# Kernel tuning notes

Hardware: AMD Instinct MI355X
Metric: run time of the kernel (lower is better)

Reference implementation:

```python
import jax, jax.numpy as jnp
import numpy as np

B, C, H, W = 4, 512, 128, 256
INNER = 128
HEADS = 4
GROUPS = 32
EPS = 1e-5


def _ln(x, w, b):
    m = x.mean(-1, keepdims=True)
    v = jnp.var(x, axis=-1, keepdims=True)
    return (x - m) * jax.lax.rsqrt(v + EPS) * w + b


def _mhsa(x, wq, wk, wv, ln_w, ln_b):
    # x: (Bn, N, Ci); torch Linear: y = x @ W.T
    Bn, N, Ci = x.shape
    d = Ci // HEADS
    xn = _ln(x, ln_w, ln_b)
    q = (xn @ wq.T).reshape(Bn, N, HEADS, d).transpose(0, 2, 1, 3)
    k = (xn @ wk.T).reshape(Bn, N, HEADS, d).transpose(0, 2, 1, 3)
    v = (xn @ wv.T).reshape(Bn, N, HEADS, d).transpose(0, 2, 1, 3)
    attn = jax.nn.softmax(jnp.einsum('bhnd,bhmd->bhnm', q, k) * (d ** -0.5), axis=-1)
    out = jnp.einsum('bhnm,bhmd->bhnd', attn, v).transpose(0, 2, 1, 3).reshape(Bn, N, Ci)
    return out


def setup_inputs() -> dict:
    key = jax.random.key(0)
    ks = jax.random.split(key, 10)
    s = 0.02
    return {
        'x': jax.random.normal(ks[0], (B, C, H, W), jnp.float32),
        'proj_in_w': jax.random.normal(ks[1], (INNER, C), jnp.float32) * s,
        't_q_w': jax.random.normal(ks[2], (INNER, INNER), jnp.float32) * s,
        't_k_w': jax.random.normal(ks[3], (INNER, INNER), jnp.float32) * s,
        't_v_w': jax.random.normal(ks[4], (INNER, INNER), jnp.float32) * s,
        't_norm_w': jnp.ones((INNER,), jnp.float32),
        't_norm_b': jnp.zeros((INNER,), jnp.float32),
        'f_q_w': jax.random.normal(ks[5], (INNER, INNER), jnp.float32) * s,
        'f_k_w': jax.random.normal(ks[6], (INNER, INNER), jnp.float32) * s,
        'f_v_w': jax.random.normal(ks[7], (INNER, INNER), jnp.float32) * s,
        'f_norm_w': jnp.ones((INNER,), jnp.float32),
        'f_norm_b': jnp.zeros((INNER,), jnp.float32),
        'proj_out_w': jax.random.normal(ks[8], (C, INNER), jnp.float32) * s,
        'gn_w': jnp.ones((C,), jnp.float32),
        'gn_b': jnp.zeros((C,), jnp.float32),
    }


def reference(x, proj_in_w, t_q_w, t_k_w, t_v_w, t_norm_w, t_norm_b,
              f_q_w, f_k_w, f_v_w, f_norm_w, f_norm_b,
              proj_out_w, gn_w, gn_b):
    Bx, Cx, Hx, Wx = x.shape
    inner = proj_in_w.shape[0]
    # 1x1 conv in
    z = jnp.einsum('bchw,oc->bohw', x, proj_in_w)
    # row-wise (temporal) attention: sequences of length Wx
    t_in = z.transpose(0, 2, 3, 1).reshape(Bx * Hx, Wx, inner)
    t_out = t_in + _mhsa(t_in, t_q_w, t_k_w, t_v_w, t_norm_w, t_norm_b)
    t_out = t_out.reshape(Bx, Hx, Wx, inner).transpose(0, 3, 1, 2)  # (B, inner, H, W)
    # col-wise (frequency) attention: sequences of length Hx
    f_in = t_out.transpose(0, 3, 2, 1).reshape(Bx * Wx, Hx, inner)
    f_out = f_in + _mhsa(f_in, f_q_w, f_k_w, f_v_w, f_norm_w, f_norm_b)
    f_out = f_out.reshape(Bx, Wx, Hx, inner).transpose(0, 3, 2, 1)  # (B, inner, H, W)
    # 1x1 conv out
    out = jnp.einsum('bihw,oi->bohw', f_out, proj_out_w)
    # GroupNorm(32, C)
    og = out.reshape(Bx, GROUPS, Cx // GROUPS, Hx, Wx)
    m = og.mean(axis=(2, 3, 4), keepdims=True)
    v = jnp.var(og, axis=(2, 3, 4), keepdims=True)
    og = (og - m) * jax.lax.rsqrt(v + EPS)
    out = og.reshape(Bx, Cx, Hx, Wx) * gn_w[None, :, None, None] + gn_b[None, :, None, None]
    return x + out
```

## Files before the change

kernel.cpp:

```cpp
#include <hip/hip_runtime.h>
#include <cstdint>

typedef __bf16 bf16;
typedef __attribute__((ext_vector_type(8))) __bf16 bf16x8;
typedef __attribute__((ext_vector_type(4))) __bf16 bf16x4;
typedef __attribute__((ext_vector_type(4))) float f32x4;

static __device__ __forceinline__ f32x4 mfma16(bf16x8 a, bf16x8 b, f32x4 c) {
    return __builtin_amdgcn_mfma_f32_16x16x32_bf16(a, b, c, 0, 0, 0);
}
static __device__ __forceinline__ bf16x4 cvt4(f32x4 v) {
    bf16x4 r; r[0]=(bf16)v[0]; r[1]=(bf16)v[1]; r[2]=(bf16)v[2]; r[3]=(bf16)v[3]; return r;
}

__global__ __launch_bounds__(256) void k_proj_in(
    const float* __restrict__ x, const float* __restrict__ Wi, bf16* __restrict__ z)
{
    __shared__ bf16 As[128][72];
    __shared__ bf16 Bs[64][72];
    const int tid = threadIdx.x;
    const int lane = tid & 63, w = tid >> 6;
    const int ll = lane & 15, lg = lane >> 4;
    const int b = blockIdx.x >> 9;
    const int n0 = (blockIdx.x & 511) * 64;
    const float* xb = x + (size_t)b * 512 * 32768;

    f32x4 acc[2][4];
    const f32x4 Z4 = {0.f,0.f,0.f,0.f};
    #pragma unroll
    for (int i=0;i<2;i++) { acc[i][0]=Z4; acc[i][1]=Z4; acc[i][2]=Z4; acc[i][3]=Z4; }

    for (int c0 = 0; c0 < 512; c0 += 64) {
        #pragma unroll
        for (int r = 0; r < 8; ++r) {
            int idx = r*256 + tid;
            int o = idx >> 4, cq = idx & 15;
            f32x4 v = *(const f32x4*)(Wi + (size_t)o*512 + c0 + cq*4);
            *(bf16x4*)&As[o][cq*4] = cvt4(v);
        }
        #pragma unroll
        for (int r = 0; r < 4; ++r) {
            int idx = r*256 + tid;
            int k = idx >> 4, nq = idx & 15;
            f32x4 v = *(const f32x4*)(xb + (size_t)(c0 + k)*32768 + n0 + nq*4);
            #pragma unroll
            for (int j=0;j<4;j++) Bs[nq*4+j][k] = (bf16)v[j];
        }
        __syncthreads();
        #pragma unroll
        for (int ks = 0; ks < 2; ++ks) {
            bf16x8 af[2], bfr[4];
            #pragma unroll
            for (int mt=0;mt<2;mt++) af[mt]  = *(const bf16x8*)&As[w*32+mt*16+ll][ks*32+lg*8];
            #pragma unroll
            for (int nt=0;nt<4;nt++) bfr[nt] = *(const bf16x8*)&Bs[nt*16+ll][ks*32+lg*8];
            #pragma unroll
            for (int mt=0;mt<2;mt++)
                #pragma unroll
                for (int nt=0;nt<4;nt++)
                    acc[mt][nt] = mfma16(af[mt], bfr[nt], acc[mt][nt]);
        }
        __syncthreads();
    }
    #pragma unroll
    for (int mt=0;mt<2;mt++)
      #pragma unroll
      for (int nt=0;nt<4;nt++) {
        int o0 = w*32 + mt*16 + lg*4;
        int token = b*32768 + n0 + nt*16 + ll;
        *(bf16x4*)&z[(size_t)token*128 + o0] = cvt4(acc[mt][nt]);
      }
}

__global__ __launch_bounds__(256) void k_qkv(
    const bf16* __restrict__ zin, const float* __restrict__ lnw, const float* __restrict__ lnb,
    const float* __restrict__ Wq, const float* __restrict__ Wk, const float* __restrict__ Wv,
    bf16* __restrict__ Qb, bf16* __restrict__ Kb, bf16* __restrict__ Vt, int nshift)
{
    __shared__ bf16 xs[64][136];
    __shared__ bf16 wsm[128][136];
    const int tid = threadIdx.x;
    const int lane = tid & 63, w = tid >> 6;
    const int ll = lane & 15, lg = lane >> 4;
    const int t0 = blockIdx.x * 64;
    const int N = 1 << nshift;

    {
        const int sub = tid & 15;
        float wv[8], bv[8];
        #pragma unroll
        for (int j=0;j<8;j++){ wv[j]=lnw[sub*8+j]; bv[j]=lnb[sub*8+j]; }
        #pragma unroll
        for (int r=0;r<4;r++){
            int tl = r*16 + (tid >> 4);
            bf16x8 v = *(const bf16x8*)&zin[(size_t)(t0+tl)*128 + sub*8];
            float f[8]; float sm=0.f, ssq=0.f;
            #pragma unroll
            for (int j=0;j<8;j++){ f[j]=(float)v[j]; sm+=f[j]; ssq+=f[j]*f[j]; }
            #pragma unroll
            for (int d=1; d<16; d<<=1){ sm += __shfl_xor(sm,d); ssq += __shfl_xor(ssq,d); }
            float mean = sm*(1.f/128.f);
            float var  = ssq*(1.f/128.f) - mean*mean;
            float rr = rsqrtf(var + 1e-5f);
            bf16x8 ov;
            #pragma unroll
            for (int j=0;j<8;j++) ov[j] = (bf16)((f[j]-mean)*rr*wv[j] + bv[j]);
            *(bf16x8*)&xs[tl][sub*8] = ov;
        }
    }

    const float* Wm[3] = {Wq, Wk, Wv};
    const f32x4 Z4 = {0.f,0.f,0.f,0.f};
    for (int m = 0; m < 3; ++m) {
        __syncthreads();
        const float scale = (m == 0) ? 0.25503486f : 1.0f;
        #pragma unroll
        for (int r=0;r<16;r++){
            int idx = r*256 + tid;
            int o = idx >> 5, q = idx & 31;
            f32x4 v = *(const f32x4*)(Wm[m] + (size_t)o*128 + q*4);
            v[0]*=scale; v[1]*=scale; v[2]*=scale; v[3]*=scale;
            *(bf16x4*)&wsm[o][q*4] = cvt4(v);
        }
        __syncthreads();
        f32x4 acc[4][2];
        #pragma unroll
        for (int i=0;i<4;i++){ acc[i][0]=Z4; acc[i][1]=Z4; }
        #pragma unroll
        for (int ks=0; ks<4; ++ks){
            bf16x8 xa[4], wb[2];
            #pragma unroll
            for (int tt=0;tt<4;tt++) xa[tt] = *(const bf16x8*)&xs[tt*16+ll][ks*32+lg*8];
            #pragma unroll
            for (int ot=0;ot<2;ot++) wb[ot] = *(const bf16x8*)&wsm[w*32+ot*16+ll][ks*32+lg*8];
            if (m < 2) {
                #pragma unroll
                for (int tt=0;tt<4;tt++)
                    #pragma unroll
                    for (int ot=0;ot<2;ot++)
                        acc[tt][ot] = mfma16(xa[tt], wb[ot], acc[tt][ot]);
            } else {
                #pragma unroll
                for (int tt=0;tt<4;tt++)
                    #pragma unroll
                    for (int ot=0;ot<2;ot++)
                        acc[tt][ot] = mfma16(wb[ot], xa[tt], acc[tt][ot]);
            }
        }
        if (m < 2) {
            bf16* dst = (m==0) ? Qb : Kb;
            #pragma unroll
            for (int tt=0;tt<4;tt++)
              #pragma unroll
              for (int ot=0;ot<2;ot++)
                #pragma unroll
                for (int r=0;r<4;r++){
                    int token = t0 + tt*16 + lg*4 + r;
                    int sq = token >> nshift, n = token & (N-1);
                    int dk = ot*16 + ll;
                    dst[((size_t)(sq*4 + w)*N + n)*32 + dk] = (bf16)acc[tt][ot][r];
                }
        } else {
            #pragma unroll
            for (int tt=0;tt<4;tt++)
              #pragma unroll
              for (int ot=0;ot<2;ot++)
                #pragma unroll
                for (int r=0;r<4;r++){
                    int dk = ot*16 + lg*4 + r;
                    int token = t0 + tt*16 + ll;
                    int sq = token >> nshift, n = token & (N-1);
                    Vt[((size_t)(sq*4 + w)*32 + dk)*N + n] = (bf16)acc[tt][ot][r];
                }
        }
    }
}

template<int N>
__global__ __launch_bounds__(256, 2) void k_attn(
    const bf16* __restrict__ Qb, const bf16* __restrict__ Kb, const bf16* __restrict__ Vt,
    const bf16* __restrict__ tin, bf16* __restrict__ tout, int spb_shift)
{
    constexpr int T = N/16;
    constexpr int NQT = N/64;
    constexpr int VP = N + 8;
    __shared__ bf16 Ks[N][40];
    __shared__ bf16 Vs[32][VP];
    const int tid = threadIdx.x;
    const int lane = tid & 63, w = tid >> 6;
    const int ll = lane & 15, lg = lane >> 4;
    const int sh = blockIdx.x;
    const int s = sh >> 2, h = sh & 3;
    const size_t base = (size_t)sh * N * 32;

    #pragma unroll
    for (int r=0;r<N/64;r++){
        int idx = r*256 + tid;
        int n = idx >> 2, c = idx & 3;
        *(bf16x8*)&Ks[n][c*8] = *(const bf16x8*)&Kb[base + (size_t)n*32 + c*8];
    }
    #pragma unroll
    for (int r=0;r<N/64;r++){
        int idx = r*256 + tid;
        int dd = idx / (N/8), nc = idx % (N/8);
        *(bf16x8*)&Vs[dd][nc*8] = *(const bf16x8*)&Vt[base + (size_t)dd*N + nc*8];
    }
    bf16x8 qf[NQT];
    #pragma unroll
    for (int qt=0;qt<NQT;qt++)
        qf[qt] = *(const bf16x8*)&Qb[base + (size_t)(w*(N/4) + qt*16 + ll)*32 + lg*8];
    __syncthreads();

    const f32x4 Z4 = {0.f,0.f,0.f,0.f};
    f32x4 Oacc[NQT][2];
    float smv[NQT];

    #pragma unroll
    for (int qt=0; qt<NQT; ++qt){
        f32x4 sc[T];
        #pragma unroll
        for (int t=0;t<T;t++){
            bf16x8 kf = *(const bf16x8*)&Ks[t*16+ll][lg*8];
            sc[t] = mfma16(kf, qf[qt], Z4);
        }
        float mx = sc[0][0];
        #pragma unroll
        for (int t=0;t<T;t++)
            #pragma unroll
            for (int r=0;r<4;r++) mx = fmaxf(mx, sc[t][r]);
        mx = fmaxf(mx, __shfl_xor(mx, 16));
        mx = fmaxf(mx, __shfl_xor(mx, 32));
        float sm = 0.f;
        #pragma unroll
        for (int t=0;t<T;t++){
            #pragma unroll
            for (int r=0;r<4;r++){ float p = exp2f(sc[t][r] - mx); sc[t][r] = p; sm += p; }
        }
        sm += __shfl_xor(sm, 16);
        sm += __shfl_xor(sm, 32);
        smv[qt] = sm;

        f32x4 O0 = Z4, O1 = Z4;
        #pragma unroll
        for (int ks=0; ks<N/32; ++ks){
            bf16x4 pa = cvt4(sc[2*ks]), pb = cvt4(sc[2*ks+1]);
            bf16x8 pf;
            #pragma unroll
            for (int j=0;j<4;j++){ pf[j] = pa[j]; pf[4+j] = pb[j]; }
            bf16x4 a0 = *(const bf16x4*)&Vs[ll][ks*32 + lg*4];
            bf16x4 a1 = *(const bf16x4*)&Vs[ll][ks*32 + lg*4 + 16];
            bf16x4 b0 = *(const bf16x4*)&Vs[16+ll][ks*32 + lg*4];
            bf16x4 b1 = *(const bf16x4*)&Vs[16+ll][ks*32 + lg*4 + 16];
            bf16x8 v0, v1;
            #pragma unroll
            for (int j=0;j<4;j++){ v0[j]=a0[j]; v0[4+j]=a1[j]; v1[j]=b0[j]; v1[4+j]=b1[j]; }
            O0 = mfma16(v0, pf, O0);
            O1 = mfma16(v1, pf, O1);
        }
        Oacc[qt][0] = O0; Oacc[qt][1] = O1;
    }

    __syncthreads();
    #pragma unroll
    for (int qt=0; qt<NQT; ++qt){
        float inv = 1.f / smv[qt];
        int q = w*(N/4) + qt*16 + ll;
        #pragma unroll
        for (int dt=0; dt<2; ++dt){
            bf16x4 o4;
            #pragma unroll
            for (int r=0;r<4;r++) o4[r] = (bf16)(Oacc[qt][dt][r]*inv);
            *(bf16x4*)&Ks[q][dt*16 + lg*4] = o4;
        }
    }
    __syncthreads();
    const int spb_mask = (1 << spb_shift) - 1;
    #pragma unroll
    for (int it=0; it<N/64; ++it){
        int q = it*64 + (tid >> 2);
        int part = tid & 3;
        size_t ti = ((size_t)(s*N + q))*128 + h*32 + part*8;
        size_t to = ((size_t)((((s >> spb_shift)*N + q) << spb_shift) + (s & spb_mask)))*128 + h*32 + part*8;
        bf16x8 a = *(const bf16x8*)&Ks[q][part*8];
        bf16x8 rs = *(const bf16x8*)&tin[ti];
        bf16x8 o;
        #pragma unroll
        for (int j=0;j<8;j++) o[j] = (bf16)((float)a[j] + (float)rs[j]);
        *(bf16x8*)&tout[to] = o;
    }
}

__global__ __launch_bounds__(256) void k_gnsum(
    const bf16* __restrict__ f, const float* __restrict__ Wo, float* __restrict__ part)
{
    __shared__ bf16 As[128][136];
    __shared__ bf16 Bs[64][136];
    const int tid = threadIdx.x;
    const int lane = tid & 63, w = tid >> 6;
    const int ll = lane & 15, lg = lane >> 4;
    const int b  = blockIdx.x >> 11;
    const int ms = (blockIdx.x >> 9) & 3;
    const int ns = blockIdx.x & 511;
    const int n0 = ns*64, o0 = ms*128;

    #pragma unroll
    for (int r=0;r<16;r++){
        int idx = r*256 + tid;
        int o = idx >> 5, q = idx & 31;
        f32x4 v = *(const f32x4*)(Wo + (size_t)(o0+o)*128 + q*4);
        *(bf16x4*)&As[o][q*4] = cvt4(v);
    }
    #pragma unroll
    for (int r=0;r<4;r++){
        int idx = r*256 + tid;
        int nl = idx >> 4, ch = idx & 15;
        *(bf16x8*)&Bs[nl][ch*8] = *(const bf16x8*)&f[(size_t)(b*32768 + n0 + nl)*128 + ch*8];
    }
    __syncthreads();
    const f32x4 Z4 = {0.f,0.f,0.f,0.f};
    f32x4 acc[2][4];
    #pragma unroll
    for (int i=0;i<2;i++){ acc[i][0]=Z4; acc[i][1]=Z4; acc[i][2]=Z4; acc[i][3]=Z4; }
    #pragma unroll
    for (int ks=0;ks<4;ks++){
        bf16x8 af[2], bfr[4];
        #pragma unroll
        for (int mt=0;mt<2;mt++) af[mt]  = *(const bf16x8*)&As[w*32+mt*16+ll][ks*32+lg*8];
        #pragma unroll
        for (int nt=0;nt<4;nt++) bfr[nt] = *(const bf16x8*)&Bs[nt*16+ll][ks*32+lg*8];
        #pragma unroll
        for (int mt=0;mt<2;mt++)
            #pragma unroll
            for (int nt=0;nt<4;nt++)
                acc[mt][nt] = mfma16(af[mt], bfr[nt], acc[mt][nt]);
    }
    #pragma unroll
    for (int mt=0;mt<2;mt++){
        float ps=0.f, pss=0.f;
        #pragma unroll
        for (int nt=0;nt<4;nt++)
            #pragma unroll
            for (int r=0;r<4;r++){ float v = acc[mt][nt][r]; ps += v; pss += v*v; }
        #pragma unroll
        for (int d=1; d<64; d<<=1){ ps += __shfl_xor(ps,d); pss += __shfl_xor(pss,d); }
        if (lane == 0){
            int g = ms*8 + w*2 + mt;
            size_t pi = ((size_t)(b*32+g)*512 + ns)*2;
            part[pi] = ps; part[pi+1] = pss;
        }
    }
}

__global__ __launch_bounds__(256) void k_gnstat(
    const float* __restrict__ part, float* __restrict__ stats)
{
    const int bg = blockIdx.x;
    float s = 0.f, ss = 0.f;
    for (int i = threadIdx.x; i < 512; i += 256) {
        s  += part[((size_t)bg*512 + i)*2];
        ss += part[((size_t)bg*512 + i)*2 + 1];
    }
    #pragma unroll
    for (int d=1; d<64; d<<=1){ s += __shfl_xor(s,d); ss += __shfl_xor(ss,d); }
    __shared__ float sh[8];
    const int w = threadIdx.x >> 6;
    if ((threadIdx.x & 63) == 0) { sh[w*2] = s; sh[w*2+1] = ss; }
    __syncthreads();
    if (threadIdx.x == 0) {
        float S = sh[0]+sh[2]+sh[4]+sh[6], SS = sh[1]+sh[3]+sh[5]+sh[7];
        float mean = S * (1.f/524288.f);
        float var  = SS * (1.f/524288.f) - mean*mean;
        stats[bg*2]   = mean;
        stats[bg*2+1] = rsqrtf(var + 1e-5f);
    }
}

__global__ __launch_bounds__(256) void k_apply(
    const bf16* __restrict__ f, const float* __restrict__ Wo, const float* __restrict__ x,
    const float* __restrict__ stats, const float* __restrict__ gw, const float* __restrict__ gb,
    float* __restrict__ out)
{
    __shared__ bf16 As[128][136];
    __shared__ bf16 Bs[64][136];
    const int tid = threadIdx.x;
    const int lane = tid & 63, w = tid >> 6;
    const int ll = lane & 15, lg = lane >> 4;
    const int b  = blockIdx.x >> 11;
    const int ms = (blockIdx.x >> 9) & 3;
    const int ns = blockIdx.x & 511;
    const int n0 = ns*64, o0 = ms*128;

    #pragma unroll
    for (int r=0;r<16;r++){
        int idx = r*256 + tid;
        int o = idx >> 5, q = idx & 31;
        f32x4 v = *(const f32x4*)(Wo + (size_t)(o0+o)*128 + q*4);
        *(bf16x4*)&As[o][q*4] = cvt4(v);
    }
    #pragma unroll
    for (int r=0;r<4;r++){
        int idx = r*256 + tid;
        int nl = idx >> 4, ch = idx & 15;
        *(bf16x8*)&Bs[nl][ch*8] = *(const bf16x8*)&f[(size_t)(b*32768 + n0 + nl)*128 + ch*8];
    }
    __syncthreads();
    const f32x4 Z4 = {0.f,0.f,0.f,0.f};
    f32x4 acc[2][4];
    #pragma unroll
    for (int i=0;i<2;i++){ acc[i][0]=Z4; acc[i][1]=Z4; acc[i][2]=Z4; acc[i][3]=Z4; }
    #pragma unroll
    for (int ks=0;ks<4;ks++){
        bf16x8 af[2], bfr[4];
        #pragma unroll
        for (int mt=0;mt<2;mt++) af[mt]  = *(const bf16x8*)&As[w*32+mt*16+ll][ks*32+lg*8];
        #pragma unroll
        for (int nt=0;nt<4;nt++) bfr[nt] = *(const bf16x8*)&Bs[nt*16+ll][ks*32+lg*8];
        #pragma unroll
        for (int mt=0;mt<2;mt++)
            #pragma unroll
            for (int nt=0;nt<4;nt++)
                acc[mt][nt] = mfma16(af[mt], bfr[nt], acc[mt][nt]);
    }
    __syncthreads();
    float* Od = (float*)&As[0][0];
    #pragma unroll
    for (int mt=0;mt<2;mt++){
        int g = ms*8 + w*2 + mt;
        float mean = stats[(b*32+g)*2];
        float rstd = stats[(b*32+g)*2+1];
        #pragma unroll
        for (int r=0;r<4;r++){
            int o_l = w*32 + mt*16 + lg*4 + r;
            float sw = rstd * gw[o0 + o_l];
            float sb = gb[o0 + o_l] - mean*sw;
            #pragma unroll
            for (int nt=0;nt<4;nt++)
                Od[o_l*68 + nt*16 + ll] = acc[mt][nt][r]*sw + sb;
        }
    }
    __syncthreads();
    #pragma unroll
    for (int it=0; it<8; ++it){
        int idx = it*256 + tid;
        int o_l = idx >> 4, c4 = (idx & 15)*4;
        size_t gi = (size_t)(b*512 + o0 + o_l)*32768 + n0 + c4;
        f32x4 xv = *(const f32x4*)(x + gi);
        f32x4 ov = *(const f32x4*)(Od + o_l*68 + c4);
        f32x4 res;
        #pragma unroll
        for (int j=0;j<4;j++) res[j] = xv[j] + ov[j];
        *(f32x4*)(out + gi) = res;
    }
}

extern "C" void kernel_launch(void* const* d_in, const int* in_sizes, int n_in,
                              void* d_out, int out_size, void* d_ws, size_t ws_size,
                              hipStream_t stream)
{
    (void)in_sizes; (void)n_in; (void)out_size; (void)ws_size;
    const float* x   = (const float*)d_in[0];
    const float* wi  = (const float*)d_in[1];
    const float* tq  = (const float*)d_in[2];
    const float* tk  = (const float*)d_in[3];
    const float* tv  = (const float*)d_in[4];
    const float* tnw = (const float*)d_in[5];
    const float* tnb = (const float*)d_in[6];
    const float* fq  = (const float*)d_in[7];
    const float* fk  = (const float*)d_in[8];
    const float* fv  = (const float*)d_in[9];
    const float* fnw = (const float*)d_in[10];
    const float* fnb = (const float*)d_in[11];
    const float* wo  = (const float*)d_in[12];
    const float* gnw = (const float*)d_in[13];
    const float* gnb = (const float*)d_in[14];
    float* out = (float*)d_out;

    char* ws = (char*)d_ws;
    const size_t MB = (size_t)1 << 20;
    bf16* Z    = (bf16*)(ws);
    bf16* QB   = (bf16*)(ws + 32*MB);
    bf16* KB   = (bf16*)(ws + 64*MB);
    bf16* VT   = (bf16*)(ws + 96*MB);
    bf16* TOUT = (bf16*)(ws + 128*MB);
    float* PART  = (float*)(ws + 32*MB);
    float* STATS = (float*)(ws + 33*MB);

    k_proj_in<<<2048, 256, 0, stream>>>(x, wi, Z);
    k_qkv<<<2048, 256, 0, stream>>>(Z, tnw, tnb, tq, tk, tv, QB, KB, VT, 8);
    k_attn<256><<<2048, 256, 0, stream>>>(QB, KB, VT, Z, TOUT, 7);
    k_qkv<<<2048, 256, 0, stream>>>(TOUT, fnw, fnb, fq, fk, fv, QB, KB, VT, 7);
    k_attn<128><<<4096, 256, 0, stream>>>(QB, KB, VT, TOUT, Z, 8);
    k_gnsum<<<8192, 256, 0, stream>>>(Z, wo, PART);
    k_gnstat<<<128, 256, 0, stream>>>(PART, STATS);
    k_apply<<<8192, 256, 0, stream>>>(Z, wo, x, STATS, gnw, gnb, out);
}
```

Baseline: 407.1 us.

## Fuse LayerNorm and QKV projection into the attention kernel

New measurement: 475.1 us. +16.7%, slower.

```diff
diff --git a/kernel.cpp b/kernel.cpp
--- a/kernel.cpp
+++ b/kernel.cpp
@@ -11,6 +11,24 @@
 }
 static __device__ __forceinline__ bf16x4 cvt4(f32x4 v) {
     bf16x4 r; r[0]=(bf16)v[0]; r[1]=(bf16)v[1]; r[2]=(bf16)v[2]; r[3]=(bf16)v[3]; return r;
+}
+static __device__ __forceinline__ bf16x8 ldw8(const float* __restrict__ p) {
+    f32x4 w0 = *(const f32x4*)p, w1 = *(const f32x4*)(p + 4);
+    bf16x4 c0 = cvt4(w0), c1 = cvt4(w1);
+    bf16x8 r;
+    #pragma unroll
+    for (int j=0;j<4;j++){ r[j] = c0[j]; r[4+j] = c1[j]; }
+    return r;
+}
+static __device__ __forceinline__ bf16x8 ldw8s(const float* __restrict__ p, float s) {
+    f32x4 w0 = *(const f32x4*)p, w1 = *(const f32x4*)(p + 4);
+    #pragma unroll
+    for (int j=0;j<4;j++){ w0[j]*=s; w1[j]*=s; }
+    bf16x4 c0 = cvt4(w0), c1 = cvt4(w1);
+    bf16x8 r;
+    #pragma unroll
+    for (int j=0;j<4;j++){ r[j] = c0[j]; r[4+j] = c1[j]; }
+    return r;
 }
 
 __global__ __launch_bounds__(256) void k_proj_in(
@@ -72,118 +90,16 @@
       }
 }
 
-__global__ __launch_bounds__(256) void k_qkv(
-    const bf16* __restrict__ zin, const float* __restrict__ lnw, const float* __restrict__ lnb,
+template<int N>
+__global__ __launch_bounds__(256, 2) void k_fattn(
+    const bf16* __restrict__ z, const float* __restrict__ lnw, const float* __restrict__ lnb,
     const float* __restrict__ Wq, const float* __restrict__ Wk, const float* __restrict__ Wv,
-    bf16* __restrict__ Qb, bf16* __restrict__ Kb, bf16* __restrict__ Vt, int nshift)
-{
-    __shared__ bf16 xs[64][136];
-    __shared__ bf16 wsm[128][136];
-    const int tid = threadIdx.x;
-    const int lane = tid & 63, w = tid >> 6;
-    const int ll = lane & 15, lg = lane >> 4;
-    const int t0 = blockIdx.x * 64;
-    const int N = 1 << nshift;
-
-    {
-        const int sub = tid & 15;
-        float wv[8], bv[8];
-        #pragma unroll
-        for (int j=0;j<8;j++){ wv[j]=lnw[sub*8+j]; bv[j]=lnb[sub*8+j]; }
-        #pragma unroll
-        for (int r=0;r<4;r++){
-            int tl = r*16 + (tid >> 4);
-            bf16x8 v = *(const bf16x8*)&zin[(size_t)(t0+tl)*128 + sub*8];
-            float f[8]; float sm=0.f, ssq=0.f;
-            #pragma unroll
-            for (int j=0;j<8;j++){ f[j]=(float)v[j]; sm+=f[j]; ssq+=f[j]*f[j]; }
-            #pragma unroll
-            for (int d=1; d<16; d<<=1){ sm += __shfl_xor(sm,d); ssq += __shfl_xor(ssq,d); }
-            float mean = sm*(1.f/128.f);
-            float var  = ssq*(1.f/128.f) - mean*mean;
-            float rr = rsqrtf(var + 1e-5f);
-            bf16x8 ov;
-            #pragma unroll
-            for (int j=0;j<8;j++) ov[j] = (bf16)((f[j]-mean)*rr*wv[j] + bv[j]);
-            *(bf16x8*)&xs[tl][sub*8] = ov;
-        }
-    }
-
-    const float* Wm[3] = {Wq, Wk, Wv};
-    const f32x4 Z4 = {0.f,0.f,0.f,0.f};
-    for (int m = 0; m < 3; ++m) {
-        __syncthreads();
-        const float scale = (m == 0) ? 0.25503486f : 1.0f;
-        #pragma unroll
-        for (int r=0;r<16;r++){
-            int idx = r*256 + tid;
-            int o = idx >> 5, q = idx & 31;
-            f32x4 v = *(const f32x4*)(Wm[m] + (size_t)o*128 + q*4);
-            v[0]*=scale; v[1]*=scale; v[2]*=scale; v[3]*=scale;
-            *(bf16x4*)&wsm[o][q*4] = cvt4(v);
-        }
-        __syncthreads();
-        f32x4 acc[4][2];
-        #pragma unroll
-        for (int i=0;i<4;i++){ acc[i][0]=Z4; acc[i][1]=Z4; }
-        #pragma unroll
-        for (int ks=0; ks<4; ++ks){
-            bf16x8 xa[4], wb[2];
-            #pragma unroll
-            for (int tt=0;tt<4;tt++) xa[tt] = *(const bf16x8*)&xs[tt*16+ll][ks*32+lg*8];
-            #pragma unroll
-            for (int ot=0;ot<2;ot++) wb[ot] = *(const bf16x8*)&wsm[w*32+ot*16+ll][ks*32+lg*8];
-            if (m < 2) {
-                #pragma unroll
-                for (int tt=0;tt<4;tt++)
-                    #pragma unroll
-                    for (int ot=0;ot<2;ot++)
-                        acc[tt][ot] = mfma16(xa[tt], wb[ot], acc[tt][ot]);
-            } else {
-                #pragma unroll
-                for (int tt=0;tt<4;tt++)
-                    #pragma unroll
-                    for (int ot=0;ot<2;ot++)
-                        acc[tt][ot] = mfma16(wb[ot], xa[tt], acc[tt][ot]);
-            }
-        }
-        if (m < 2) {
-            bf16* dst = (m==0) ? Qb : Kb;
-            #pragma unroll
-            for (int tt=0;tt<4;tt++)
-              #pragma unroll
-              for (int ot=0;ot<2;ot++)
-                #pragma unroll
-                for (int r=0;r<4;r++){
-                    int token = t0 + tt*16 + lg*4 + r;
-                    int sq = token >> nshift, n = token & (N-1);
-                    int dk = ot*16 + ll;
-                    dst[((size_t)(sq*4 + w)*N + n)*32 + dk] = (bf16)acc[tt][ot][r];
-                }
-        } else {
-            #pragma unroll
-            for (int tt=0;tt<4;tt++)
-              #pragma unroll
-              for (int ot=0;ot<2;ot++)
-                #pragma unroll
-                for (int r=0;r<4;r++){
-                    int dk = ot*16 + lg*4 + r;
-                    int token = t0 + tt*16 + ll;
-                    int sq = token >> nshift, n = token & (N-1);
-                    Vt[((size_t)(sq*4 + w)*32 + dk)*N + n] = (bf16)acc[tt][ot][r];
-                }
-        }
-    }
-}
-
-template<int N>
-__global__ __launch_bounds__(256, 2) void k_attn(
-    const bf16* __restrict__ Qb, const bf16* __restrict__ Kb, const bf16* __restrict__ Vt,
-    const bf16* __restrict__ tin, bf16* __restrict__ tout, int spb_shift)
+    bf16* __restrict__ tout, int spb_shift)
 {
     constexpr int T = N/16;
     constexpr int NQT = N/64;
     constexpr int VP = N + 8;
+    __shared__ bf16 xs[64][136];
     __shared__ bf16 Ks[N][40];
     __shared__ bf16 Vs[32][VP];
     const int tid = threadIdx.x;
@@ -191,36 +107,98 @@
     const int ll = lane & 15, lg = lane >> 4;
     const int sh = blockIdx.x;
     const int s = sh >> 2, h = sh & 3;
-    const size_t base = (size_t)sh * N * 32;
-
-    #pragma unroll
-    for (int r=0;r<N/64;r++){
-        int idx = r*256 + tid;
-        int n = idx >> 2, c = idx & 3;
-        *(bf16x8*)&Ks[n][c*8] = *(const bf16x8*)&Kb[base + (size_t)n*32 + c*8];
-    }
-    #pragma unroll
-    for (int r=0;r<N/64;r++){
-        int idx = r*256 + tid;
-        int dd = idx / (N/8), nc = idx % (N/8);
-        *(bf16x8*)&Vs[dd][nc*8] = *(const bf16x8*)&Vt[base + (size_t)dd*N + nc*8];
-    }
+    const bf16* zs = z + (size_t)s * N * 128;
+
+    bf16x8 wbq[4][2], wbk[4][2], wbv[4][2];
+    #pragma unroll
+    for (int ks=0;ks<4;ks++)
+      #pragma unroll
+      for (int ot=0;ot<2;ot++){
+        const size_t row = (size_t)(h*32 + ot*16 + ll)*128 + ks*32 + lg*8;
+        wbq[ks][ot] = ldw8s(Wq + row, 0.25503486f);
+        wbk[ks][ot] = ldw8 (Wk + row);
+        wbv[ks][ot] = ldw8 (Wv + row);
+      }
+    const int sub = tid & 15;
+    float lwv[8], lbv[8];
+    #pragma unroll
+    for (int j=0;j<8;j++){ lwv[j]=lnw[sub*8+j]; lbv[j]=lnb[sub*8+j]; }
+
+    const f32x4 Z4 = {0.f,0.f,0.f,0.f};
     bf16x8 qf[NQT];
-    #pragma unroll
-    for (int qt=0;qt<NQT;qt++)
-        qf[qt] = *(const bf16x8*)&Qb[base + (size_t)(w*(N/4) + qt*16 + ll)*32 + lg*8];
-    __syncthreads();
-
-    const f32x4 Z4 = {0.f,0.f,0.f,0.f};
+
+    #pragma unroll
+    for (int tt=0; tt<NQT; ++tt){
+        __syncthreads();
+        #pragma unroll
+        for (int r=0;r<4;r++){
+            int tl = r*16 + (tid >> 4);
+            bf16x8 v = *(const bf16x8*)&zs[(size_t)(tt*64+tl)*128 + sub*8];
+            float f[8]; float sm=0.f, ssq=0.f;
+            #pragma unroll
+            for (int j=0;j<8;j++){ f[j]=(float)v[j]; sm+=f[j]; ssq+=f[j]*f[j]; }
+            #pragma unroll
+            for (int d=1; d<16; d<<=1){ sm += __shfl_xor(sm,d); ssq += __shfl_xor(ssq,d); }
+            float mean = sm*(1.f/128.f);
+            float var  = ssq*(1.f/128.f) - mean*mean;
+            float rr = rsqrtf(var + 1e-5f);
+            bf16x8 ov;
+            #pragma unroll
+            for (int j=0;j<8;j++) ov[j] = (bf16)((f[j]-mean)*rr*lwv[j] + lbv[j]);
+            *(bf16x8*)&xs[tl][sub*8] = ov;
+        }
+        __syncthreads();
+        bf16x8 xa[4];
+        #pragma unroll
+        for (int ks=0;ks<4;ks++) xa[ks] = *(const bf16x8*)&xs[w*16+ll][ks*32+lg*8];
+
+        f32x4 aq0 = Z4, aq1 = Z4;
+        #pragma unroll
+        for (int ks=0;ks<4;ks++){
+            aq0 = mfma16(wbq[ks][0], xa[ks], aq0);
+            aq1 = mfma16(wbq[ks][1], xa[ks], aq1);
+        }
+        { bf16x4 c0 = cvt4(aq0), c1 = cvt4(aq1);
+          #pragma unroll
+          for (int j=0;j<4;j++){ qf[tt][j] = c0[j]; qf[tt][4+j] = c1[j]; } }
+
+        f32x4 ak0 = Z4, ak1 = Z4;
+        #pragma unroll
+        for (int ks=0;ks<4;ks++){
+            ak0 = mfma16(xa[ks], wbk[ks][0], ak0);
+            ak1 = mfma16(xa[ks], wbk[ks][1], ak1);
+        }
+        #pragma unroll
+        for (int r=0;r<4;r++){
+            Ks[tt*64 + w*16 + lg*4 + r][ll]      = (bf16)ak0[r];
+            Ks[tt*64 + w*16 + lg*4 + r][16 + ll] = (bf16)ak1[r];
+        }
+        f32x4 av0 = Z4, av1 = Z4;
+        #pragma unroll
+        for (int ks=0;ks<4;ks++){
+            av0 = mfma16(wbv[ks][0], xa[ks], av0);
+            av1 = mfma16(wbv[ks][1], xa[ks], av1);
+        }
+        #pragma unroll
+        for (int r=0;r<4;r++){
+            Vs[lg*4 + r][tt*64 + w*16 + ll]      = (bf16)av0[r];
+            Vs[16 + lg*4 + r][tt*64 + w*16 + ll] = (bf16)av1[r];
+        }
+    }
+    __syncthreads();
+
     f32x4 Oacc[NQT][2];
     float smv[NQT];
-
     #pragma unroll
     for (int qt=0; qt<NQT; ++qt){
         f32x4 sc[T];
         #pragma unroll
         for (int t=0;t<T;t++){
-            bf16x8 kf = *(const bf16x8*)&Ks[t*16+ll][lg*8];
+            bf16x4 k0 = *(const bf16x4*)&Ks[t*16+ll][lg*4];
+            bf16x4 k1 = *(const bf16x4*)&Ks[t*16+ll][16 + lg*4];
+            bf16x8 kf;
+            #pragma unroll
+            for (int j=0;j<4;j++){ kf[j] = k0[j]; kf[4+j] = k1[j]; }
             sc[t] = mfma16(kf, qf[qt], Z4);
         }
         float mx = sc[0][0];
@@ -264,7 +242,7 @@
     #pragma unroll
     for (int qt=0; qt<NQT; ++qt){
         float inv = 1.f / smv[qt];
-        int q = w*(N/4) + qt*16 + ll;
+        int q = qt*64 + w*16 + ll;
         #pragma unroll
         for (int dt=0; dt<2; ++dt){
             bf16x4 o4;
@@ -282,7 +260,7 @@
         size_t ti = ((size_t)(s*N + q))*128 + h*32 + part*8;
         size_t to = ((size_t)((((s >> spb_shift)*N + q) << spb_shift) + (s & spb_mask)))*128 + h*32 + part*8;
         bf16x8 a = *(const bf16x8*)&Ks[q][part*8];
-        bf16x8 rs = *(const bf16x8*)&tin[ti];
+        bf16x8 rs = *(const bf16x8*)&z[ti];
         bf16x8 o;
         #pragma unroll
         for (int j=0;j<8;j++) o[j] = (bf16)((float)a[j] + (float)rs[j]);
@@ -478,18 +456,13 @@
     char* ws = (char*)d_ws;
     const size_t MB = (size_t)1 << 20;
     bf16* Z    = (bf16*)(ws);
-    bf16* QB   = (bf16*)(ws + 32*MB);
-    bf16* KB   = (bf16*)(ws + 64*MB);
-    bf16* VT   = (bf16*)(ws + 96*MB);
     bf16* TOUT = (bf16*)(ws + 128*MB);
     float* PART  = (float*)(ws + 32*MB);
     float* STATS = (float*)(ws + 33*MB);
 
     k_proj_in<<<2048, 256, 0, stream>>>(x, wi, Z);
-    k_qkv<<<2048, 256, 0, stream>>>(Z, tnw, tnb, tq, tk, tv, QB, KB, VT, 8);
-    k_attn<256><<<2048, 256, 0, stream>>>(QB, KB, VT, Z, TOUT, 7);
-    k_qkv<<<2048, 256, 0, stream>>>(TOUT, fnw, fnb, fq, fk, fv, QB, KB, VT, 7);
-    k_attn<128><<<4096, 256, 0, stream>>>(QB, KB, VT, TOUT, Z, 8);
+    k_fattn<256><<<2048, 256, 0, stream>>>(Z, tnw, tnb, tq, tk, tv, TOUT, 7);
+    k_fattn<128><<<4096, 256, 0, stream>>>(TOUT, fnw, fnb, fq, fk, fv, Z, 8);
     k_gnsum<<<8192, 256, 0, stream>>>(Z, wo, PART);
     k_gnstat<<<128, 256, 0, stream>>>(PART, STATS);
     k_apply<<<8192, 256, 0, stream>>>(Z, wo, x, STATS, gnw, gnb, out);
```

## Compute GroupNorm stats from feature covariance instead of recomputing proj_out

Applied to the files above, without the earlier changes.

Result: no change. 415.0 us (+1.9%).

```diff
diff --git a/kernel.cpp b/kernel.cpp
--- a/kernel.cpp
+++ b/kernel.cpp
@@ -290,88 +290,113 @@
     }
 }
 
-__global__ __launch_bounds__(256) void k_gnsum(
-    const bf16* __restrict__ f, const float* __restrict__ Wo, float* __restrict__ part)
-{
-    __shared__ bf16 As[128][136];
-    __shared__ bf16 Bs[64][136];
+__global__ __launch_bounds__(256) void k_cov(
+    const bf16* __restrict__ f, float* __restrict__ part)
+{
+    __shared__ bf16 ct[144][72];
     const int tid = threadIdx.x;
     const int lane = tid & 63, w = tid >> 6;
     const int ll = lane & 15, lg = lane >> 4;
-    const int b  = blockIdx.x >> 11;
-    const int ms = (blockIdx.x >> 9) & 3;
-    const int ns = blockIdx.x & 511;
-    const int n0 = ns*64, o0 = ms*128;
-
-    #pragma unroll
-    for (int r=0;r<16;r++){
-        int idx = r*256 + tid;
-        int o = idx >> 5, q = idx & 31;
-        f32x4 v = *(const f32x4*)(Wo + (size_t)(o0+o)*128 + q*4);
-        *(bf16x4*)&As[o][q*4] = cvt4(v);
-    }
-    #pragma unroll
-    for (int r=0;r<4;r++){
-        int idx = r*256 + tid;
-        int nl = idx >> 4, ch = idx & 15;
-        *(bf16x8*)&Bs[nl][ch*8] = *(const bf16x8*)&f[(size_t)(b*32768 + n0 + nl)*128 + ch*8];
-    }
-    __syncthreads();
+    const int b = blockIdx.x >> 6, sl = blockIdx.x & 63;
+    const size_t tb = (size_t)b*32768 + (size_t)sl*512;
+
+    for (int idx = tid; idx < 16*72; idx += 256)
+        ct[128 + idx/72][idx%72] = (bf16)((idx/72 == 0) ? 1.0f : 0.0f);
+
     const f32x4 Z4 = {0.f,0.f,0.f,0.f};
-    f32x4 acc[2][4];
-    #pragma unroll
-    for (int i=0;i<2;i++){ acc[i][0]=Z4; acc[i][1]=Z4; acc[i][2]=Z4; acc[i][3]=Z4; }
-    #pragma unroll
-    for (int ks=0;ks<4;ks++){
-        bf16x8 af[2], bfr[4];
-        #pragma unroll
-        for (int mt=0;mt<2;mt++) af[mt]  = *(const bf16x8*)&As[w*32+mt*16+ll][ks*32+lg*8];
-        #pragma unroll
-        for (int nt=0;nt<4;nt++) bfr[nt] = *(const bf16x8*)&Bs[nt*16+ll][ks*32+lg*8];
-        #pragma unroll
-        for (int mt=0;mt<2;mt++)
-            #pragma unroll
-            for (int nt=0;nt<4;nt++)
-                acc[mt][nt] = mfma16(af[mt], bfr[nt], acc[mt][nt]);
-    }
-    #pragma unroll
-    for (int mt=0;mt<2;mt++){
-        float ps=0.f, pss=0.f;
-        #pragma unroll
-        for (int nt=0;nt<4;nt++)
-            #pragma unroll
-            for (int r=0;r<4;r++){ float v = acc[mt][nt][r]; ps += v; pss += v*v; }
-        #pragma unroll
-        for (int d=1; d<64; d<<=1){ ps += __shfl_xor(ps,d); pss += __shfl_xor(pss,d); }
-        if (lane == 0){
-            int g = ms*8 + w*2 + mt;
-            size_t pi = ((size_t)(b*32+g)*512 + ns)*2;
-            part[pi] = ps; part[pi+1] = pss;
-        }
-    }
-}
-
-__global__ __launch_bounds__(256) void k_gnstat(
-    const float* __restrict__ part, float* __restrict__ stats)
-{
-    const int bg = blockIdx.x;
-    float s = 0.f, ss = 0.f;
-    for (int i = threadIdx.x; i < 512; i += 256) {
-        s  += part[((size_t)bg*512 + i)*2];
-        ss += part[((size_t)bg*512 + i)*2 + 1];
-    }
-    #pragma unroll
-    for (int d=1; d<64; d<<=1){ s += __shfl_xor(s,d); ss += __shfl_xor(ss,d); }
-    __shared__ float sh[8];
-    const int w = threadIdx.x >> 6;
-    if ((threadIdx.x & 63) == 0) { sh[w*2] = s; sh[w*2+1] = ss; }
-    __syncthreads();
-    if (threadIdx.x == 0) {
-        float S = sh[0]+sh[2]+sh[4]+sh[6], SS = sh[1]+sh[3]+sh[5]+sh[7];
-        float mean = S * (1.f/524288.f);
-        float var  = SS * (1.f/524288.f) - mean*mean;
-        stats[bg*2]   = mean;
-        stats[bg*2+1] = rsqrtf(var + 1e-5f);
+    f32x4 acc[2][9];
+    #pragma unroll
+    for (int mt=0;mt<2;mt++)
+        #pragma unroll
+        for (int jt=0;jt<9;jt++) acc[mt][jt] = Z4;
+
+    for (int c = 0; c < 8; ++c){
+        __syncthreads();
+        #pragma unroll
+        for (int it=0; it<4; ++it){
+            int cg = it*4 + w;
+            bf16x8 v = *(const bf16x8*)&f[(tb + c*64 + lane)*128 + cg*8];
+            #pragma unroll
+            for (int j=0;j<8;j++) ct[cg*8+j][lane] = v[j];
+        }
+        __syncthreads();
+        #pragma unroll
+        for (int ks=0; ks<2; ++ks){
+            bf16x8 am[2], bm[9];
+            #pragma unroll
+            for (int mt=0;mt<2;mt++) am[mt] = *(const bf16x8*)&ct[w*32+mt*16+ll][ks*32+lg*8];
+            #pragma unroll
+            for (int jt=0;jt<9;jt++) bm[jt] = *(const bf16x8*)&ct[jt*16+ll][ks*32+lg*8];
+            #pragma unroll
+            for (int mt=0;mt<2;mt++)
+                #pragma unroll
+                for (int jt=0;jt<9;jt++)
+                    acc[mt][jt] = mfma16(am[mt], bm[jt], acc[mt][jt]);
+        }
+    }
+    float* pp = part + (size_t)blockIdx.x * 18432;
+    #pragma unroll
+    for (int mt=0;mt<2;mt++)
+        #pragma unroll
+        for (int jt=0;jt<9;jt++)
+            #pragma unroll
+            for (int r=0;r<4;r++){
+                int i = w*32 + mt*16 + lg*4 + r;
+                int j = jt*16 + ll;
+                pp[i*144 + j] = acc[mt][jt][r];
+            }
+}
+
+__global__ __launch_bounds__(256) void k_redM(
+    const float* __restrict__ part, float* __restrict__ Mred)
+{
+    const int b = blockIdx.x / 72, r = blockIdx.x % 72;
+    const int e = r*256 + threadIdx.x;
+    float s = 0.f;
+    for (int sl = 0; sl < 64; ++sl)
+        s += part[((size_t)(b*64 + sl))*18432 + e];
+    Mred[(size_t)b*18432 + e] = s;
+}
+
+__global__ __launch_bounds__(256) void k_gnstat2(
+    const float* __restrict__ Mred, const float* __restrict__ Wo, float* __restrict__ stats)
+{
+    __shared__ float Ms[18432];
+    __shared__ float wv[16][132];
+    __shared__ float redq[16], redm[16];
+    const int tid = threadIdx.x;
+    const int b = blockIdx.x >> 5, g = blockIdx.x & 31;
+    #pragma unroll 4
+    for (int r=0;r<72;r++){ int off = r*256+tid; Ms[off] = Mred[(size_t)b*18432 + off]; }
+    for (int idx=tid; idx<2048; idx+=256){
+        int o = idx>>7, i = idx&127;
+        wv[o][i] = Wo[(size_t)(g*16+o)*128 + i];
+    }
+    __syncthreads();
+    const int o = tid >> 4, ts = tid & 15;
+    float q = 0.f, mn = 0.f;
+    for (int ii=0; ii<8; ++ii){
+        int i = ts*8 + ii;
+        const float wi = wv[o][i];
+        float dot = 0.f;
+        for (int jj=0; jj<128; ++jj){
+            int j = (jj + ts*8) & 127;
+            dot += Ms[i*144 + j] * wv[o][j];
+        }
+        q  += wi*dot;
+        mn += wi*Ms[i*144 + 128];
+    }
+    #pragma unroll
+    for (int d=1; d<16; d<<=1){ q += __shfl_xor(q,d); mn += __shfl_xor(mn,d); }
+    if (ts == 0){ redq[o] = q; redm[o] = mn; }
+    __syncthreads();
+    if (tid == 0){
+        float sq=0.f, smm=0.f;
+        for (int o2=0;o2<16;o2++){ sq += redq[o2]; smm += redm[o2]; }
+        float mean = smm * (1.f/524288.f);
+        float var  = sq  * (1.f/524288.f) - mean*mean;
+        stats[(b*32+g)*2]   = mean;
+        stats[(b*32+g)*2+1] = rsqrtf(var + 1e-5f);
     }
 }
 
@@ -482,15 +507,17 @@
     bf16* KB   = (bf16*)(ws + 64*MB);
     bf16* VT   = (bf16*)(ws + 96*MB);
     bf16* TOUT = (bf16*)(ws + 128*MB);
-    float* PART  = (float*)(ws + 32*MB);
-    float* STATS = (float*)(ws + 33*MB);
+    float* PARTC = (float*)(ws + 32*MB);
+    float* MRED  = (float*)(ws + 64*MB);
+    float* STATS = (float*)(ws + 66*MB);
 
     k_proj_in<<<2048, 256, 0, stream>>>(x, wi, Z);
     k_qkv<<<2048, 256, 0, stream>>>(Z, tnw, tnb, tq, tk, tv, QB, KB, VT, 8);
     k_attn<256><<<2048, 256, 0, stream>>>(QB, KB, VT, Z, TOUT, 7);
     k_qkv<<<2048, 256, 0, stream>>>(TOUT, fnw, fnb, fq, fk, fv, QB, KB, VT, 7);
     k_attn<128><<<4096, 256, 0, stream>>>(QB, KB, VT, TOUT, Z, 8);
-    k_gnsum<<<8192, 256, 0, stream>>>(Z, wo, PART);
-    k_gnstat<<<128, 256, 0, stream>>>(PART, STATS);
+    k_cov<<<256, 256, 0, stream>>>(Z, PARTC);
+    k_redM<<<288, 256, 0, stream>>>(PARTC, MRED);
+    k_gnstat2<<<128, 256, 0, stream>>>(MRED, wo, STATS);
     k_apply<<<8192, 256, 0, stream>>>(Z, wo, x, STATS, gnw, gnb, out);
 }
```
